# Performance work log

Hardware: AMD Instinct MI355X
Metric: run time of the kernel (lower is better)

The kernel has to match this reference:

```python
import jax, jax.numpy as jnp
import numpy as np

KER = 3          # CausalPool1d kernel
PAD_VAL = 1e-8   # left-pad value
K = 3            # harmonic_num
H = 4200         # rows of integral matrix
F = 321          # frequency bins


def setup_inputs() -> dict:
    key = jax.random.key(0)
    k1, k2, k3 = jax.random.split(key, 3)
    mag = jax.random.uniform(k1, (8, 2, F, 1000), dtype=jnp.float32)          # B,C,F,T (magnitude >= 0)
    integral_m = jax.random.normal(k2, (H, F), dtype=jnp.float32)             # buffer integral_m (squeezed)
    harmonic_loc = jax.random.normal(k3, (H, F), dtype=jnp.float32)           # buffer harmonic_loc (squeezed)
    return {"mag": mag, "integral_m": integral_m, "harmonic_loc": harmonic_loc, "freq_dim": F}


def reference(mag, integral_m, harmonic_loc, freq_dim):
    # harmonic_nominee: (B,C,H,T) = integral_m @ mag
    nominee = jnp.einsum('hf,bcft->bcht', integral_m, mag)
    # topk over the H axis (torch dim=-2); lax.top_k works on last axis -> move H last
    _, pos = jax.lax.top_k(jnp.moveaxis(nominee, 2, -1), K)  # (B,C,T,K), descending like torch
    pos = jnp.moveaxis(pos, -1, 2).astype(jnp.float32)       # (B,C,K,T)
    # CausalPool1d: left-pad (KER-1) with 1e-8, avg over window KER, stride 1 (vectorized over K)
    xp = jnp.pad(pos, ((0, 0), (0, 0), (0, 0), (KER - 1, 0)), constant_values=PAD_VAL)
    T = pos.shape[-1]
    choose = ((xp[..., 0:T] + xp[..., 1:T + 1] + xp[..., 2:T + 2]) / KER).astype(jnp.int32)  # (B,C,K,T)
    # gather harmonic_loc rows and accumulate over the K harmonics
    gathered = harmonic_loc[choose]          # (B,C,K,T,F)
    summed = gathered.sum(axis=2)            # (B,C,T,F)
    # (B,C,F,T) threshold mask, matching torch's (x > 0).float()
    out = (jnp.swapaxes(summed, -1, -2) > 0).astype(jnp.float32)
    return out
```

## Files before the change

### kernel.cpp

```cpp
#include <hip/hip_runtime.h>
#include <math.h>

#define F_DIM 321
#define H_DIM 4200
#define T_DIM 1000
#define NBC   16
#define KTOP  3
#define PADV  1e-8f

#define BM 128
#define BN 128
#define BK 16
#define LDA 16
#define LDB 128
#define NHT 33
#define NKT 20

typedef float v4f __attribute__((ext_vector_type(4)));
typedef __attribute__((address_space(3))) uint32_t lds_u32;
typedef const __attribute__((address_space(1))) uint32_t glb_u32;

__device__ __forceinline__ void ins3(float v, int i,
                                     float& v0, float& v1, float& v2,
                                     int& i0, int& i1, int& i2) {
  if (v > v0)      { v2 = v1; i2 = i1; v1 = v0; i1 = i0; v0 = v; i0 = i; }
  else if (v > v1) { v2 = v1; i2 = i1; v1 = v;  i1 = i; }
  else if (v > v2) { v2 = v;  i2 = i; }
}

__global__ __launch_bounds__(256)
void hi_k1_gemm_top3(const float* __restrict__ mag,
                     const float* __restrict__ im,
                     float* __restrict__ wv, int* __restrict__ wi,
                     int nsplit) {
  const int tid = threadIdx.x;
  const int tx = tid & 15;
  const int ty = tid >> 4;
  const int wv_ = tid >> 6;
  const int lam = tid & 63;
  const int t0 = blockIdx.x * BN;
  const int bc = blockIdx.y;
  const int sp = blockIdx.z;
  const int ht_begin = (sp * NHT) / nsplit;
  const int ht_end   = ((sp + 1) * NHT) / nsplit;
  const int row0 = ty * 8;
  const int xsw = (ty & 3) << 2;

  __shared__ __align__(16) float As[2][BM * LDA];
  __shared__ __align__(16) float Bs[2][BK * LDB];
  __shared__ float mv[4 * BN * KTOP];
  __shared__ int   mi[4 * BN * KTOP];

  const float* magbc = mag + (size_t)bc * F_DIM * T_DIM;

  auto stageA = [&](int buf, int nh0, int nk0) {
#pragma unroll
    for (int i = 0; i < 8; ++i) {
      int row = wv_ * 32 + i * 4 + (lam >> 4);
      int gh = nh0 + row;
      gh = (gh < H_DIM) ? gh : (H_DIM - 1);
      int key = ((row >> 3) & 3) << 2;
      const float* src = im + (size_t)gh * F_DIM + nk0 + ((lam & 15) ^ key);
      __builtin_amdgcn_global_load_lds(
          (glb_u32*)src,
          (lds_u32*)&As[buf][(wv_ * 32 + i * 4) * LDA], 4, 0, 0);
    }
  };
  auto stageB = [&](int buf, int nk0) {
#pragma unroll
    for (int i = 0; i < 2; ++i) {
      int kr = wv_ * 4 + i * 2 + (lam >> 5);
      const float* src = magbc + (size_t)(nk0 + kr) * T_DIM + t0 + (lam & 31) * 4;
      __builtin_amdgcn_global_load_lds(
          (glb_u32*)src,
          (lds_u32*)&Bs[buf][(wv_ * 4 + i * 2) * LDB], 16, 0, 0);
    }
  };

  float gv0 = -INFINITY, gv1 = -INFINITY, gv2 = -INFINITY;
  int   gi0 = 0, gi1 = 0, gi2 = 0;

  int cur = 0;
  stageA(0, ht_begin * BM, 0);
  stageB(0, 0);
  __syncthreads();

  for (int ht = ht_begin; ht < ht_end; ++ht) {
    const int h0 = ht * BM;
    float acc[8][8];
#pragma unroll
    for (int r = 0; r < 8; ++r)
#pragma unroll
      for (int c = 0; c < 8; ++c) acc[r][c] = 0.f;

    for (int kt = 0; kt < NKT; ++kt) {
      bool have_next = true;
      int nh0 = h0, nk0 = (kt + 1) * BK;
      if (kt == NKT - 1) {
        if (ht + 1 < ht_end) { nh0 = h0 + BM; nk0 = 0; }
        else have_next = false;
      }
      if (have_next) { stageA(cur ^ 1, nh0, nk0); stageB(cur ^ 1, nk0); }

#pragma unroll 1
      for (int g = 0; g < 4; ++g) {
        v4f Bv[8];
#pragma unroll
        for (int kk = 0; kk < 4; ++kk) {
          Bv[kk * 2]     = *(const v4f*)(&Bs[cur][(g * 4 + kk) * LDB + tx * 4]);
          Bv[kk * 2 + 1] = *(const v4f*)(&Bs[cur][(g * 4 + kk) * LDB + 64 + tx * 4]);
        }
#pragma unroll
        for (int r = 0; r < 8; ++r) {
          const v4f Ar = *(const v4f*)(&As[cur][(row0 + r) * LDA + ((g * 4) ^ xsw)]);
#pragma unroll
          for (int kk = 0; kk < 4; ++kk)
#pragma unroll
            for (int c = 0; c < 4; ++c) {
              acc[r][c]     = fmaf(Ar[kk], Bv[kk * 2][c],     acc[r][c]);
              acc[r][c + 4] = fmaf(Ar[kk], Bv[kk * 2 + 1][c], acc[r][c + 4]);
            }
        }
      }

      __syncthreads();
      cur ^= 1;
    }

    {
      float bt[8];
#pragma unroll
      for (int c = 0; c < 8; ++c) {
        int gt = t0 + ((c < 4) ? (tx * 4 + c) : (64 + tx * 4 + c - 4));
        bt[c] = (gt < T_DIM) ? magbc[(size_t)(F_DIM - 1) * T_DIM + gt] : 0.f;
      }
#pragma unroll
      for (int r = 0; r < 8; ++r) {
        int gh = h0 + row0 + r;
        float a = (gh < H_DIM) ? im[(size_t)gh * F_DIM + (F_DIM - 1)] : 0.f;
#pragma unroll
        for (int c = 0; c < 8; ++c) acc[r][c] = fmaf(a, bt[c], acc[r][c]);
      }
    }

#pragma unroll
    for (int c = 0; c < 8; ++c) {
      const int col = (c < 4) ? (tx * 4 + c) : (64 + tx * 4 + c - 4);
      float v0 = -INFINITY, v1 = -INFINITY, v2 = -INFINITY;
      int   i0 = 0, i1 = 0, i2 = 0;
#pragma unroll
      for (int r = 0; r < 8; ++r) {
        int gh = h0 + row0 + r;
        float v = (gh < H_DIM) ? acc[r][c] : -INFINITY;
        ins3(v, gh, v0, v1, v2, i0, i1, i2);
      }
#pragma unroll
      for (int s = 0; s < 2; ++s) {
        const int off = 16 << s;
        float ov0 = __shfl_down(v0, off);
        float ov1 = __shfl_down(v1, off);
        float ov2 = __shfl_down(v2, off);
        int   oi0 = __shfl_down(i0, off);
        int   oi1 = __shfl_down(i1, off);
        int   oi2 = __shfl_down(i2, off);
        ins3(ov0, oi0, v0, v1, v2, i0, i1, i2);
        ins3(ov1, oi1, v0, v1, v2, i0, i1, i2);
        ins3(ov2, oi2, v0, v1, v2, i0, i1, i2);
      }
      if ((ty & 3) == 0) {
        mv[(wv_ * BN + col) * 3 + 0] = v0;
        mv[(wv_ * BN + col) * 3 + 1] = v1;
        mv[(wv_ * BN + col) * 3 + 2] = v2;
        mi[(wv_ * BN + col) * 3 + 0] = i0;
        mi[(wv_ * BN + col) * 3 + 1] = i1;
        mi[(wv_ * BN + col) * 3 + 2] = i2;
      }
    }
    __syncthreads();
    if (tid < BN) {
#pragma unroll
      for (int w = 0; w < 4; ++w)
#pragma unroll
        for (int j = 0; j < 3; ++j) {
          float v = mv[(w * BN + tid) * 3 + j];
          int   i = mi[(w * BN + tid) * 3 + j];
          ins3(v, i, gv0, gv1, gv2, gi0, gi1, gi2);
        }
    }
  }

  if (tid < BN) {
    int t = t0 + tid;
    if (t < T_DIM) {
      size_t base = ((size_t)(bc * nsplit + sp) * KTOP) * T_DIM + t;
      wv[base]             = gv0;
      wv[base + T_DIM]     = gv1;
      wv[base + 2 * T_DIM] = gv2;
      wi[base]             = gi0;
      wi[base + T_DIM]     = gi1;
      wi[base + 2 * T_DIM] = gi2;
    }
  }
}

__global__ __launch_bounds__(256, 4)
void hi_k3_pool_gather(const float* __restrict__ wv, const int* __restrict__ wi,
                       const float* __restrict__ hl, float* __restrict__ out,
                       int nsplit) {
  const int tid = threadIdx.x;
  const int t0 = blockIdx.x * 64;
  const int bc = blockIdx.y;

  __shared__ float pos_lds[66 * KTOP];
  __shared__ int   rows[64 * KTOP];
  __shared__ float S[64 * 65];

  if (tid < 66) {
    int t = t0 - 2 + tid;
    float p0 = PADV, p1 = PADV, p2 = PADV;
    if (t >= 0 && t < T_DIM) {
      float v0 = -INFINITY, v1 = -INFINITY, v2 = -INFINITY;
      int i0 = 0, i1 = 0, i2 = 0;
      for (int sp = 0; sp < nsplit; ++sp)
        for (int j = 0; j < KTOP; ++j) {
          size_t idx = ((size_t)(bc * nsplit + sp) * KTOP + j) * T_DIM + t;
          ins3(wv[idx], wi[idx], v0, v1, v2, i0, i1, i2);
        }
      p0 = (float)i0; p1 = (float)i1; p2 = (float)i2;
    }
    pos_lds[tid * KTOP + 0] = p0;
    pos_lds[tid * KTOP + 1] = p1;
    pos_lds[tid * KTOP + 2] = p2;
  }
  __syncthreads();
  if (tid < 64) {
#pragma unroll
    for (int k = 0; k < KTOP; ++k) {
      float s = (pos_lds[tid * KTOP + k] + pos_lds[(tid + 1) * KTOP + k])
                + pos_lds[(tid + 2) * KTOP + k];
      rows[tid * KTOP + k] = (int)(s / 3.0f);
    }
  }
  __syncthreads();

  const int w = tid >> 6, lane = tid & 63;
  for (int fc = 0; fc < 6; ++fc) {
    const int f0 = fc * 64;
    for (int i = 0; i < 16; ++i) {
      int tl = w * 16 + i;
      int r0 = rows[tl * KTOP + 0];
      int r1 = rows[tl * KTOP + 1];
      int r2 = rows[tl * KTOP + 2];
      int f = f0 + lane;
      float s = 0.f;
      if (f < F_DIM)
        s = (hl[(size_t)r0 * F_DIM + f] + hl[(size_t)r1 * F_DIM + f])
            + hl[(size_t)r2 * F_DIM + f];
      S[tl * 65 + lane] = s;
    }
    __syncthreads();
#pragma unroll
    for (int i = 0; i < 16; ++i) {
      int e = tid + 256 * i;
      int fl = e >> 6, tl = e & 63;
      int f = f0 + fl, t = t0 + tl;
      if (f < F_DIM && t < T_DIM)
        out[((size_t)bc * F_DIM + f) * T_DIM + t] = (S[tl * 65 + fl] > 0.f) ? 1.f : 0.f;
    }
    __syncthreads();
  }
}

extern "C" void kernel_launch(void* const* d_in, const int* in_sizes, int n_in,
                              void* d_out, int out_size, void* d_ws, size_t ws_size,
                              hipStream_t stream) {
  const float* mag = (const float*)d_in[0];
  const float* im  = (const float*)d_in[1];
  const float* hl  = (const float*)d_in[2];
  float* out = (float*)d_out;

  int nsplit = (ws_size >= (size_t)NBC * 8 * KTOP * T_DIM * 8) ? 8 : 4;
  float* wv = (float*)d_ws;
  int*   wi = (int*)d_ws + (size_t)NBC * nsplit * KTOP * T_DIM;

  dim3 g1((T_DIM + BN - 1) / BN, NBC, nsplit);
  hipLaunchKernelGGL(hi_k1_gemm_top3, g1, dim3(256), 0, stream, mag, im, wv, wi, nsplit);

  dim3 g3((T_DIM + 63) / 64, NBC);
  hipLaunchKernelGGL(hi_k3_pool_gather, g3, dim3(256), 0, stream, wv, wi, hl, out, nsplit);
}
```

Measured before the change: 1.044 ms.

## Prefetch two stages ahead with explicit vmcnt waits in GEMM top-3 kernel

Restructures the double-buffered GEMM mainloop so each tile is loaded two iterations ahead, using a flattened tile index across H tiles and K steps. Explicit s_waitcnt vmcnt(10) and raw s_barrier calls replace __syncthreads, letting the next tile's loads stay in flight while the current one is consumed. The goal is to hide global-to-LDS latency better. The cost is two barriers per K step, plus an extra sync after each H tile's top-3 merge. Correctness depends on the hard-coded vmcnt count matching the number of issued loads.

```diff
diff --git a/kernel.cpp b/kernel.cpp
--- a/kernel.cpp
+++ b/kernel.cpp
@@ -43,6 +43,8 @@
   const int sp = blockIdx.z;
   const int ht_begin = (sp * NHT) / nsplit;
   const int ht_end   = ((sp + 1) * NHT) / nsplit;
+  const int nht = ht_end - ht_begin;
+  const int NT = nht * NKT;
   const int row0 = ty * 8;
   const int xsw = (ty & 3) << 2;
 
@@ -76,17 +78,21 @@
           (lds_u32*)&Bs[buf][(wv_ * 4 + i * 2) * LDB], 16, 0, 0);
     }
   };
+  auto nh0_of = [&](int i) { return (ht_begin + i / NKT) * BM; };
+  auto nk0_of = [&](int i) { return (i % NKT) * BK; };
 
   float gv0 = -INFINITY, gv1 = -INFINITY, gv2 = -INFINITY;
   int   gi0 = 0, gi1 = 0, gi2 = 0;
 
+  stageA(0, nh0_of(0), nk0_of(0)); stageB(0, nk0_of(0));
+  stageA(1, nh0_of(1), nk0_of(1)); stageB(1, nk0_of(1));
+  asm volatile("s_waitcnt vmcnt(10)" ::: "memory");
+  __builtin_amdgcn_s_barrier();
+  __builtin_amdgcn_sched_barrier(0);
+
   int cur = 0;
-  stageA(0, ht_begin * BM, 0);
-  stageB(0, 0);
-  __syncthreads();
-
-  for (int ht = ht_begin; ht < ht_end; ++ht) {
-    const int h0 = ht * BM;
+  for (int ht = 0; ht < nht; ++ht) {
+    const int h0 = (ht_begin + ht) * BM;
     float acc[8][8];
 #pragma unroll
     for (int r = 0; r < 8; ++r)
@@ -94,13 +100,7 @@
       for (int c = 0; c < 8; ++c) acc[r][c] = 0.f;
 
     for (int kt = 0; kt < NKT; ++kt) {
-      bool have_next = true;
-      int nh0 = h0, nk0 = (kt + 1) * BK;
-      if (kt == NKT - 1) {
-        if (ht + 1 < ht_end) { nh0 = h0 + BM; nk0 = 0; }
-        else have_next = false;
-      }
-      if (have_next) { stageA(cur ^ 1, nh0, nk0); stageB(cur ^ 1, nk0); }
+      const int i = ht * NKT + kt;
 
 #pragma unroll 1
       for (int g = 0; g < 4; ++g) {
@@ -123,7 +123,20 @@
         }
       }
 
-      __syncthreads();
+      asm volatile("" ::: "memory");
+      __builtin_amdgcn_s_barrier();
+      __builtin_amdgcn_sched_barrier(0);
+
+      if (i + 2 < NT) {
+        stageA(cur, nh0_of(i + 2), nk0_of(i + 2));
+        stageB(cur, nk0_of(i + 2));
+        asm volatile("s_waitcnt vmcnt(10)" ::: "memory");
+      } else {
+        asm volatile("s_waitcnt vmcnt(0)" ::: "memory");
+      }
+      asm volatile("" ::: "memory");
+      __builtin_amdgcn_s_barrier();
+      __builtin_amdgcn_sched_barrier(0);
       cur ^= 1;
     }
 
@@ -187,6 +200,7 @@
           ins3(v, i, gv0, gv1, gv2, gi0, gi1, gi2);
         }
     }
+    __syncthreads();
   }
 
   if (tid < BN) {
```

After: 1.026 ms. No clear change (-1.7%).
